# Performance work log

Measured on AMD Instinct MI355X. Metric: run time of the kernel, lower is better.

Reference implementation:

```python
import jax, jax.numpy as jnp
import numpy as np

B, G1, S, GS, D, T, H = 64, 128, 32, 16, 384, 10, 6
HD = D // H
SCALE = HD ** -0.5
GELU = lambda v: jax.nn.gelu(v, approximate=False)


def layer_norm(v, g, b, eps=1e-5):
    m = jnp.mean(v, -1, keepdims=True)
    s = jnp.mean((v - m) ** 2, -1, keepdims=True)
    return (v - m) * jax.lax.rsqrt(s + eps) * g + b


def mha(xn, qkv_w, proj_w, proj_b):
    Bc, N, C = xn.shape
    qkv = (xn @ qkv_w.T).reshape(Bc, N, 3, H, HD)
    qkv = jnp.transpose(qkv, (2, 0, 3, 1, 4))  # [3,B,H,N,hd]
    q, k, v = qkv[0], qkv[1], qkv[2]
    attn = jax.nn.softmax(jnp.einsum('bhnd,bhmd->bhnm', q, k) * SCALE, axis=-1)
    o = jnp.einsum('bhnm,bhmd->bhnd', attn, v)
    o = jnp.transpose(o, (0, 2, 1, 3)).reshape(Bc, N, C)
    return o @ proj_w.T + proj_b, attn


def propagate(xyz1, xyz2, points1, points2, de_neighbors):
    # squared pairwise distances [B,N,S]
    d = jnp.sum((xyz1[:, :, None, :] - xyz2[:, None, :, :]) ** 2, -1)
    order = jnp.argsort(d, axis=-1)[..., :de_neighbors]
    dists = jnp.take_along_axis(d, order, axis=-1)
    w = 1.0 / (dists + 1e-8)
    w = w / jnp.sum(w, -1, keepdims=True)
    gathered = jax.vmap(lambda p, i: p[i])(points2, order)  # [B,N,de,Dp]
    interp = jnp.sum(gathered * w[..., None], axis=2)
    return points1 + 0.3 * interp


def setup_inputs() -> dict:
    key = jax.random.key(0)
    ks = iter(jax.random.split(key, 64))
    rn = lambda sh, sc=1.0: jax.random.normal(next(ks), sh, jnp.float32) * sc
    w = 0.02
    inp = dict(
        x=rn((B, G1 + 1, D)),
        mask=jnp.zeros((B, G1, G1), jnp.float32),
        center1=rn((B, G1, 3)),
        center2=rn((B, S, 3)),
        neighborhood=rn((B, S, GS, 3)),
        idx=jax.random.randint(next(ks), (B * S * GS,), 0, B * (G1 + T)),
        center_idx=jax.random.randint(next(ks), (B * S,), 0, B * (G1 + T)),
        group_size=GS,
        layer_id=3,
        ln1_g=jnp.ones((D,)), ln1_b=jnp.zeros((D,)),
        ln2_g=jnp.ones((D,)), ln2_b=jnp.zeros((D,)),
        qkv_w=rn((3 * D, D), w), proj_w=rn((D, D), w), proj_b=jnp.zeros((D,)),
        fc1_w=rn((4 * D, D), w), fc1_b=jnp.zeros((4 * D,)),
        fc2_w=rn((D, 4 * D), w), fc2_b=jnp.zeros((D,)),
        ad_down_w=rn((16, D), w), ad_down_b=jnp.zeros((16,)),
        ad_up_w=rn((D, 16), w), ad_up_b=jnp.zeros((D,)),
        ad1_down_w=rn((16, D), w), ad1_down_b=jnp.zeros((16,)),
        ad1_up_w=rn((D, 16), w), ad1_up_b=jnp.zeros((D,)),
        prompt_emb=rn((T, D), w),
        bn_g=jnp.ones((D,)), bn_b=jnp.zeros((D,)),
        bn_mean=jnp.zeros((D,)), bn_var=jnp.ones((D,)),
        qkv1_w=rn((3 * D, D), w), proj1_w=rn((D, D), w), proj1_b=jnp.zeros((D,)),
        ln3_g=jnp.ones((D,)), ln3_b=jnp.zeros((D,)),
    )
    return inp


def block_forward(x, mask, center1, center2, neighborhood, idx, center_idx,
                  group_size, layer_id,
                  ln1_g, ln1_b, ln2_g, ln2_b, qkv_w, proj_w, proj_b,
                  fc1_w, fc1_b, fc2_w, fc2_b,
                  ad_down_w, ad_down_b, ad_up_w, ad_up_b,
                  ad1_down_w, ad1_down_b, ad1_up_w, ad1_up_b,
                  prompt_emb, bn_g, bn_b, bn_mean, bn_var,
                  qkv1_w, proj1_w, proj1_b, ln3_g, ln3_b):
    Bc = x.shape[0]
    # mask padding (built but unused by Attention, matching the source)
    # layer_id <= 5 branch (layer_id=3)
    prompt = jnp.broadcast_to(prompt_emb[None], (Bc, T, D))  # dropout off (eval)
    x = jnp.concatenate([x[:, :1], prompt, x[:, 1:]], axis=1)  # [B, 1+T+G1, D]
    x_fn, attn_weight = mha(layer_norm(x, ln1_g, ln1_b), qkv_w, proj_w, proj_b)
    x = x_fn + x
    xn2 = layer_norm(x, ln2_g, ln2_b)
    x_fn = GELU(xn2 @ fc1_w.T + fc1_b) @ fc2_w.T + fc2_b
    # AdapterSuper_f: bottleneck down-GELU-up (no internal residual)
    ad = GELU(x_fn @ ad_down_w.T + ad_down_b) @ ad_up_w.T + ad_up_b
    x = 0.7 * ad + x_fn + x
    prompt = x[:, 1:T + 1]
    x = jnp.concatenate([x[:, :1], x[:, T + 1:]], axis=1)  # [B, 1+G1, D]
    cls_x = x[:, 0]
    x = x[:, 1:]  # [B, G1, D]
    G = G1 + T
    prompt_x = jnp.concatenate([prompt, x], axis=1).reshape(Bc * G, D)
    x_neigh = prompt_x[idx].reshape(Bc * S, group_size, D)
    x_centers = prompt_x[center_idx].reshape(Bc, S, D)
    _ = neighborhood / (jnp.std(neighborhood) + 1e-5)  # dead in source
    # local attention over each neighborhood group
    xn3 = layer_norm(x_neigh, ln3_g, ln3_b)
    attn1_out, _a = mha(xn3, qkv1_w, proj1_w, proj1_b)
    x_neigh = attn1_out + x_neigh
    # pooling: max over group, then eval BatchNorm1d + GELU over channel dim
    lc = jnp.max(x_neigh.reshape(Bc, S, group_size, D), axis=2)  # [B,S,D]
    lc = (lc - bn_mean) * jax.lax.rsqrt(bn_var + 1e-5) * bn_g + bn_b
    lc = GELU(lc)
    vis_x = lc + 0.3 * x_centers
    x = propagate(center1, center2, x, vis_x, S)
    x = jnp.concatenate([cls_x[:, None], prompt, x], axis=1)  # [B, 1+T+G1, D]
    # AdapterSuper: bottleneck with internal residual
    x = GELU(x @ ad1_down_w.T + ad1_down_b) @ ad1_up_w.T + ad1_up_b + x
    x = jnp.concatenate([x[:, :1], x[:, T + 1:]], axis=1)  # [B, 1+G1, D]
    return x, attn_weight


def reference(x, mask, center1, center2, neighborhood, idx, center_idx,
              group_size, layer_id,
              ln1_g, ln1_b, ln2_g, ln2_b, qkv_w, proj_w, proj_b,
              fc1_w, fc1_b, fc2_w, fc2_b,
              ad_down_w, ad_down_b, ad_up_w, ad_up_b,
              ad1_down_w, ad1_down_b, ad1_up_w, ad1_up_b,
              prompt_emb, bn_g, bn_b, bn_mean, bn_var,
              qkv1_w, proj1_w, proj1_b, ln3_g, ln3_b):
    return block_forward(x, mask, center1, center2, neighborhood, idx, center_idx,
                         group_size, layer_id,
                         ln1_g, ln1_b, ln2_g, ln2_b, qkv_w, proj_w, proj_b,
                         fc1_w, fc1_b, fc2_w, fc2_b,
                         ad_down_w, ad_down_b, ad_up_w, ad_up_b,
                         ad1_down_w, ad1_down_b, ad1_up_w, ad1_up_b,
                         prompt_emb, bn_g, bn_b, bn_mean, bn_var,
                         qkv1_w, proj1_w, proj1_b, ln3_g, ln3_b)
```

## Files before the change

kernel.cpp:

```cpp
#include <hip/hip_runtime.h>
#include <hip/hip_bf16.h>

typedef __hip_bfloat16 bf16;
typedef __attribute__((ext_vector_type(8))) short short8;
typedef __attribute__((ext_vector_type(4))) float f32x4;

#define DEV static __device__ __forceinline__

DEV float b2f(bf16 v) { return __bfloat162float(v); }
DEV bf16 f2b(float v) { return __float2bfloat16(v); }
DEV unsigned short f2bu(float v) { return __builtin_bit_cast(unsigned short, __float2bfloat16(v)); }
DEV float u2f(unsigned short u) { return __uint_as_float(((unsigned int)u) << 16); }
DEV float gelu(float x) { return 0.5f * x * (1.0f + erff(x * 0.70710678118654752f)); }

#define BB 64
#define NT 139
#define DD 384
#define TT 10
#define HH 6
#define GG 138
#define M1 8896
#define MG 8832
#define NGRP 2048
#define SCALE 0.125f

#define XC_OFF   0UL
#define VIS_OFF  13664256UL
#define XNB_OFF  16809984UL
#define XFN_OFF  23642112UL
#define T16_OFF  37306368UL
#define BIG1_OFF 37875712UL
#define BIG2_OFF 58372096UL
#define ATT_OFF  XNB_OFF
#define WB_OFF   85700608UL

#define WB_QKV   0
#define WB_PROJ  442368
#define WB_FC1   589824
#define WB_FC2   1179648
#define WB_QKV1  1769472
#define WB_PROJ1 2211840
#define WB_TOTAL 2359296

#define OUT_X 3170304

DEV float4 ld4(const float* p) { return *(const float4*)p; }
DEV float4 ld4(const bf16* p) {
    ushort4 u = *(const ushort4*)p;
    return make_float4(u2f(u.x), u2f(u.y), u2f(u.z), u2f(u.w));
}
DEV void stc(float* p, float v) { *p = v; }
DEV void stc(bf16* p, float v) { *p = f2b(v); }

__global__ __launch_bounds__(256) void k_wconv(const float* __restrict__ w0, const float* __restrict__ w1,
                                               const float* __restrict__ w2, const float* __restrict__ w3,
                                               const float* __restrict__ w4, const float* __restrict__ w5,
                                               bf16* __restrict__ dst) {
    int i4 = (blockIdx.x * 256 + threadIdx.x) * 4;
    if (i4 >= WB_TOTAL) return;
    const float* s; int off;
    if (i4 < WB_PROJ)       { s = w0; off = WB_QKV; }
    else if (i4 < WB_FC1)   { s = w1; off = WB_PROJ; }
    else if (i4 < WB_FC2)   { s = w2; off = WB_FC1; }
    else if (i4 < WB_QKV1)  { s = w3; off = WB_FC2; }
    else if (i4 < WB_PROJ1) { s = w4; off = WB_QKV1; }
    else                    { s = w5; off = WB_PROJ1; }
    float4 v = *(const float4*)(s + (i4 - off));
    ushort4 u;
    u.x = f2bu(v.x); u.y = f2bu(v.y); u.z = f2bu(v.z); u.w = f2bu(v.w);
    *(ushort4*)((unsigned short*)dst + i4) = u;
}

__global__ __launch_bounds__(256) void k_build_xc(const float* __restrict__ x,
                                                  const float* __restrict__ pe,
                                                  float* __restrict__ xc) {
    int i = blockIdx.x * 256 + threadIdx.x;
    if (i >= M1 * DD) return;
    int d = i % DD, r = i / DD, n = r % NT, b = r / NT;
    float v;
    if (n == 0)        v = x[(b * 129) * DD + d];
    else if (n <= TT)  v = pe[(n - 1) * DD + d];
    else               v = x[(b * 129 + n - TT) * DD + d];
    xc[i] = v;
}

__global__ __launch_bounds__(128) void k_layernorm(const float* __restrict__ src, bf16* __restrict__ dst,
                                                   const float* __restrict__ g, const float* __restrict__ bta,
                                                   int mode) {
    int r = blockIdx.x;
    int srow = r;
    if (mode) srow = (r / GG) * NT + 1 + (r % GG);
    const float* p = src + (size_t)srow * DD;
    int t = threadIdx.x;
    float v0 = p[t], v1 = p[t + 128], v2 = p[t + 256];
    __shared__ float red[4];
    float s = v0 + v1 + v2;
    for (int off = 32; off; off >>= 1) s += __shfl_down(s, off, 64);
    if ((t & 63) == 0) red[t >> 6] = s;
    __syncthreads();
    float mean = (red[0] + red[1]) * (1.0f / 384.0f);
    float d0 = v0 - mean, d1 = v1 - mean, d2 = v2 - mean;
    float s2 = d0 * d0 + d1 * d1 + d2 * d2;
    for (int off = 32; off; off >>= 1) s2 += __shfl_down(s2, off, 64);
    if ((t & 63) == 0) red[2 + (t >> 6)] = s2;
    __syncthreads();
    float rstd = rsqrtf((red[2] + red[3]) * (1.0f / 384.0f) + 1e-5f);
    bf16* q = dst + (size_t)r * DD;
    q[t]       = f2b(d0 * rstd * g[t]       + bta[t]);
    q[t + 128] = f2b(d1 * rstd * g[t + 128] + bta[t + 128]);
    q[t + 256] = f2b(d2 * rstd * g[t + 256] + bta[t + 256]);
}

template <typename TC>
__global__ __launch_bounds__(256) void mf_gemm(const bf16* __restrict__ A, const bf16* __restrict__ W,
                                               const float* __restrict__ bias, const float* __restrict__ res,
                                               TC* __restrict__ C, int M, int N, int K, int act) {
    __shared__ bf16 As[64][72];
    __shared__ bf16 Ws[64][72];
    int t = threadIdx.x;
    int m0 = blockIdx.y * 64, n0 = blockIdx.x * 64;
    int lane = t & 63, wv = t >> 6;
    int wm = (wv >> 1) * 32, wn = (wv & 1) * 32;
    int fr = lane & 15, fq = lane >> 4;
    int sr = t >> 2, sc = (t & 3) * 16;
    const bf16* pa = A + (size_t)(m0 + sr) * K + sc;
    const bf16* pw = W + (size_t)(n0 + sr) * K + sc;
    uint4 ra0 = *(const uint4*)pa;
    uint4 ra1 = *(const uint4*)(pa + 8);
    uint4 rw0 = *(const uint4*)pw;
    uint4 rw1 = *(const uint4*)(pw + 8);
    f32x4 acc[2][2] = {};
    int k0 = 0;
    for (;;) {
        *(uint4*)&As[sr][sc] = ra0; *(uint4*)&As[sr][sc + 8] = ra1;
        *(uint4*)&Ws[sr][sc] = rw0; *(uint4*)&Ws[sr][sc + 8] = rw1;
        __syncthreads();
        k0 += 64;
        bool more = (k0 < K);
        if (more) {
            ra0 = *(const uint4*)(pa + k0); ra1 = *(const uint4*)(pa + k0 + 8);
            rw0 = *(const uint4*)(pw + k0); rw1 = *(const uint4*)(pw + k0 + 8);
        }
#pragma unroll
        for (int ks = 0; ks < 2; ++ks) {
            short8 a0 = *(const short8*)&As[wm + fr][ks * 32 + fq * 8];
            short8 a1 = *(const short8*)&As[wm + 16 + fr][ks * 32 + fq * 8];
            short8 b0 = *(const short8*)&Ws[wn + fr][ks * 32 + fq * 8];
            short8 b1 = *(const short8*)&Ws[wn + 16 + fr][ks * 32 + fq * 8];
            acc[0][0] = __builtin_amdgcn_mfma_f32_16x16x32_bf16(a0, b0, acc[0][0], 0, 0, 0);
            acc[0][1] = __builtin_amdgcn_mfma_f32_16x16x32_bf16(a0, b1, acc[0][1], 0, 0, 0);
            acc[1][0] = __builtin_amdgcn_mfma_f32_16x16x32_bf16(a1, b0, acc[1][0], 0, 0, 0);
            acc[1][1] = __builtin_amdgcn_mfma_f32_16x16x32_bf16(a1, b1, acc[1][1], 0, 0, 0);
        }
        if (!more) break;
        __syncthreads();
    }
#pragma unroll
    for (int i = 0; i < 2; ++i) {
#pragma unroll
        for (int r = 0; r < 4; ++r) {
            int row = m0 + wm + i * 16 + fq * 4 + r;
            size_t ro = (size_t)row * N;
#pragma unroll
            for (int j = 0; j < 2; ++j) {
                int col = n0 + wn + j * 16 + fr;
                float c = acc[i][j][r];
                if (bias) c += bias[col];
                if (act == 1) c = gelu(c);
                if (res) c += res[ro + col];
                stc(&C[ro + col], c);
            }
        }
    }
}

#define BM 64
#define BN 64
#define BKK 16
template <typename TA, typename TC>
__global__ __launch_bounds__(256) void k_gemm(const TA* __restrict__ A, const float* __restrict__ W,
                                              const float* __restrict__ bias, const float* __restrict__ res,
                                              TC* __restrict__ C, int M, int N, int K, int act) {
    __shared__ float As[BKK][BM + 4];
    __shared__ float Wsm[BKK][BN + 4];
    int t = threadIdx.x;
    int tx = t & 15, ty = t >> 4;
    int m0 = blockIdx.y * BM, n0 = blockIdx.x * BN;
    int lr = t >> 2;
    int lk = (t & 3) * 4;
    float acc[4][4] = {};
    for (int k0 = 0; k0 < K; k0 += BKK) {
        float4 av = ld4(A + (size_t)(m0 + lr) * K + k0 + lk);
        As[lk + 0][lr] = av.x; As[lk + 1][lr] = av.y;
        As[lk + 2][lr] = av.z; As[lk + 3][lr] = av.w;
        int wrr = n0 + lr;
        float4 wv = make_float4(0.f, 0.f, 0.f, 0.f);
        if (wrr < N) wv = ld4(W + (size_t)wrr * K + k0 + lk);
        Wsm[lk + 0][lr] = wv.x; Wsm[lk + 1][lr] = wv.y;
        Wsm[lk + 2][lr] = wv.z; Wsm[lk + 3][lr] = wv.w;
        __syncthreads();
#pragma unroll
        for (int k = 0; k < BKK; ++k) {
            float a0 = As[k][ty * 4 + 0], a1 = As[k][ty * 4 + 1];
            float a2 = As[k][ty * 4 + 2], a3 = As[k][ty * 4 + 3];
            float b0 = Wsm[k][tx * 4 + 0], b1 = Wsm[k][tx * 4 + 1];
            float b2 = Wsm[k][tx * 4 + 2], b3 = Wsm[k][tx * 4 + 3];
            acc[0][0] += a0 * b0; acc[0][1] += a0 * b1; acc[0][2] += a0 * b2; acc[0][3] += a0 * b3;
            acc[1][0] += a1 * b0; acc[1][1] += a1 * b1; acc[1][2] += a1 * b2; acc[1][3] += a1 * b3;
            acc[2][0] += a2 * b0; acc[2][1] += a2 * b1; acc[2][2] += a2 * b2; acc[2][3] += a2 * b3;
            acc[3][0] += a3 * b0; acc[3][1] += a3 * b1; acc[3][2] += a3 * b2; acc[3][3] += a3 * b3;
        }
        __syncthreads();
    }
#pragma unroll
    for (int i = 0; i < 4; ++i) {
        int m = m0 + ty * 4 + i;
        size_t ro = (size_t)m * N;
#pragma unroll
        for (int j = 0; j < 4; ++j) {
            int n = n0 + tx * 4 + j;
            if (n < N) {
                float c = acc[i][j];
                if (bias) c += bias[n];
                if (act == 1) c = gelu(c);
                if (res) c += res[ro + n];
                stc(&C[ro + n], c);
            }
        }
    }
}

__global__ __launch_bounds__(256) void k_attn1(const bf16* __restrict__ qkv, bf16* __restrict__ o_out,
                                               float* __restrict__ attn_out) {
    int bh = blockIdx.x;
    int b = bh / HH, h = bh % HH;
    __shared__ unsigned short Kl[144][72];
    __shared__ unsigned short Vt[64][160];
    __shared__ unsigned short Pl[4][16][160];
    int t = threadIdx.x;
    int lane = t & 63, wv = t >> 6;
    int fr = lane & 15, fq = lane >> 4;
    const unsigned short* q16 = (const unsigned short*)qkv;
    size_t base = (size_t)b * NT * 1152;

    uint4 z4 = make_uint4(0, 0, 0, 0);
    for (int i = t * 8; i < 64 * 160; i += 2048) *(uint4*)(&Vt[0][0] + i) = z4;
    for (int i = t * 8; i < 4 * 16 * 160; i += 2048) *(uint4*)(&Pl[0][0][0] + i) = z4;
    for (int i = t; i < 144 * 8; i += 256) {
        int row = i >> 3, ch = (i & 7) * 8;
        uint4 v = z4;
        if (row < NT) v = *(const uint4*)(q16 + base + row * 1152 + 384 + h * 64 + ch);
        *(uint4*)&Kl[row][ch] = v;
    }
    for (int i = t; i < NT * 16; i += 256) {
        int m = i >> 4, dq = (i & 15) * 4;
        ushort4 v = *(const ushort4*)(q16 + base + m * 1152 + 768 + h * 64 + dq);
        Vt[dq + 0][m] = v.x; Vt[dq + 1][m] = v.y;
        Vt[dq + 2][m] = v.z; Vt[dq + 3][m] = v.w;
    }
    __syncthreads();

    for (int nt = wv; nt < 9; nt += 4) {
        int n0 = nt * 16;
        int arow = n0 + fr; if (arow > NT - 1) arow = NT - 1;
        const unsigned short* qp = q16 + base + (size_t)arow * 1152 + h * 64 + fq * 8;
        short8 a0 = *(const short8*)qp;
        short8 a1 = *(const short8*)(qp + 32);
        f32x4 s[9] = {};
#pragma unroll
        for (int mt = 0; mt < 9; ++mt) {
            short8 b0 = *(const short8*)&Kl[mt * 16 + fr][fq * 8];
            short8 b1 = *(const short8*)&Kl[mt * 16 + fr][32 + fq * 8];
            s[mt] = __builtin_amdgcn_mfma_f32_16x16x32_bf16(a0, b0, s[mt], 0, 0, 0);
            s[mt] = __builtin_amdgcn_mfma_f32_16x16x32_bf16(a1, b1, s[mt], 0, 0, 0);
        }
#pragma unroll
        for (int r = 0; r < 4; ++r) {
            float e[9];
            float mx = -1e30f;
#pragma unroll
            for (int mt = 0; mt < 9; ++mt) {
                int col = mt * 16 + fr;
                float v = (col < NT) ? s[mt][r] * SCALE : -1e30f;
                e[mt] = v;
                mx = fmaxf(mx, v);
            }
#pragma unroll
            for (int off = 1; off < 16; off <<= 1) mx = fmaxf(mx, __shfl_xor(mx, off, 64));
            float sm = 0.f;
#pragma unroll
            for (int mt = 0; mt < 9; ++mt) { e[mt] = __expf(e[mt] - mx); sm += e[mt]; }
#pragma unroll
            for (int off = 1; off < 16; off <<= 1) sm += __shfl_xor(sm, off, 64);
            float inv = 1.0f / sm;
            int n = n0 + fq * 4 + r;
            bool nv = n < NT;
            size_t ab = ((size_t)(b * HH + h) * NT + n) * NT;
#pragma unroll
            for (int mt = 0; mt < 9; ++mt) {
                float p = e[mt] * inv;
                int col = mt * 16 + fr;
                if (nv && col < NT) attn_out[ab + col] = p;
                Pl[wv][fq * 4 + r][col] = f2bu(p);
            }
        }
        __syncthreads();
        f32x4 oac[4] = {};
#pragma unroll
        for (int ks = 0; ks < 5; ++ks) {
            short8 ap = *(const short8*)&Pl[wv][fr][ks * 32 + fq * 8];
#pragma unroll
            for (int dt = 0; dt < 4; ++dt) {
                short8 bv = *(const short8*)&Vt[dt * 16 + fr][ks * 32 + fq * 8];
                oac[dt] = __builtin_amdgcn_mfma_f32_16x16x32_bf16(ap, bv, oac[dt], 0, 0, 0);
            }
        }
#pragma unroll
        for (int dt = 0; dt < 4; ++dt)
#pragma unroll
            for (int r = 0; r < 4; ++r) {
                int n = n0 + fq * 4 + r;
                if (n < NT)
                    o_out[((size_t)(b * NT + n)) * DD + h * 64 + dt * 16 + fr] = f2b(oac[dt][r]);
            }
    }
}

__global__ __launch_bounds__(64) void k_attn2(const bf16* __restrict__ qkv, const int* __restrict__ idx,
                                              bf16* __restrict__ o1) {
    int g = blockIdx.x;
    __shared__ unsigned short Vt2[64][40];
    __shared__ unsigned short P2[16][40];
    __shared__ int ridx[16];
    int t = threadIdx.x;
    int fr = t & 15, fq = t >> 4;
    const unsigned short* q16 = (const unsigned short*)qkv;
    if (t < 16) ridx[t] = idx[g * 16 + t];
    uint4 z4 = make_uint4(0, 0, 0, 0);
    for (int i = t * 8; i < 64 * 40; i += 512) *(uint4*)(&Vt2[0][0] + i) = z4;
    for (int i = t * 8; i < 16 * 40; i += 512) *(uint4*)(&P2[0][0] + i) = z4;
    __syncthreads();
    size_t qb = (size_t)ridx[fr] * 1152;
    for (int h = 0; h < HH; ++h) {
        for (int i = t; i < 256; i += 64) {
            int m = i >> 4, dq = (i & 15) * 4;
            ushort4 v = *(const ushort4*)(q16 + (size_t)ridx[m] * 1152 + 768 + h * 64 + dq);
            Vt2[dq + 0][m] = v.x; Vt2[dq + 1][m] = v.y;
            Vt2[dq + 2][m] = v.z; Vt2[dq + 3][m] = v.w;
        }
        __syncthreads();
        const unsigned short* qp = q16 + qb + h * 64 + fq * 8;
        const unsigned short* kp = q16 + qb + 384 + h * 64 + fq * 8;
        short8 a0 = *(const short8*)qp;
        short8 a1 = *(const short8*)(qp + 32);
        short8 b0 = *(const short8*)kp;
        short8 b1 = *(const short8*)(kp + 32);
        f32x4 s = {};
        s = __builtin_amdgcn_mfma_f32_16x16x32_bf16(a0, b0, s, 0, 0, 0);
        s = __builtin_amdgcn_mfma_f32_16x16x32_bf16(a1, b1, s, 0, 0, 0);
#pragma unroll
        for (int r = 0; r < 4; ++r) {
            float v = s[r] * SCALE;
            float mx = v;
#pragma unroll
            for (int off = 1; off < 16; off <<= 1) mx = fmaxf(mx, __shfl_xor(mx, off, 64));
            float e = __expf(v - mx), sm = e;
#pragma unroll
            for (int off = 1; off < 16; off <<= 1) sm += __shfl_xor(sm, off, 64);
            P2[fq * 4 + r][fr] = f2bu(e / sm);
        }
        __syncthreads();
        short8 ap = *(const short8*)&P2[fr][fq * 8];
        f32x4 oac[4] = {};
#pragma unroll
        for (int dt = 0; dt < 4; ++dt) {
            short8 bv = *(const short8*)&Vt2[dt * 16 + fr][fq * 8];
            oac[dt] = __builtin_amdgcn_mfma_f32_16x16x32_bf16(ap, bv, oac[dt], 0, 0, 0);
        }
#pragma unroll
        for (int dt = 0; dt < 4; ++dt)
#pragma unroll
            for (int r = 0; r < 4; ++r)
                o1[((size_t)(g * 16 + fq * 4 + r)) * DD + h * 64 + dt * 16 + fr] = f2b(oac[dt][r]);
        __syncthreads();
    }
}

__global__ __launch_bounds__(128) void k_ad_combine(const float* __restrict__ t16, const float* __restrict__ upw,
                                                    const float* __restrict__ upb, const float* __restrict__ xfn,
                                                    float* xc) {
    int r = blockIdx.x, t = threadIdx.x;
    __shared__ float tl[16];
    if (t < 16) tl[t] = t16[r * 16 + t];
    __syncthreads();
    for (int d = t; d < DD; d += 128) {
        float acc = 0.f;
#pragma unroll
        for (int c = 0; c < 4; ++c) {
            float4 u = *(const float4*)(upw + d * 16 + c * 4);
            acc += tl[c * 4 + 0] * u.x + tl[c * 4 + 1] * u.y
                 + tl[c * 4 + 2] * u.z + tl[c * 4 + 3] * u.w;
        }
        acc += upb[d];
        size_t i = (size_t)r * DD + d;
        xc[i] += 0.7f * acc + xfn[i];
    }
}

__global__ __launch_bounds__(128) void k_groupmax(const bf16* __restrict__ att, const float* __restrict__ xc,
                                                  const int* __restrict__ idx, const int* __restrict__ cidx,
                                                  const float* __restrict__ bg, const float* __restrict__ bb,
                                                  const float* __restrict__ bmean, const float* __restrict__ bvar,
                                                  float* __restrict__ vis) {
    int g = blockIdx.x, t = threadIdx.x;
    __shared__ int rows[16];
    __shared__ int crow;
    if (t < 16) { int r = idx[g * 16 + t]; rows[t] = (r / GG) * NT + 1 + (r % GG); }
    if (t == 16) { int r = cidx[g]; crow = (r / GG) * NT + 1 + (r % GG); }
    __syncthreads();
    for (int d = t; d < DD; d += 128) {
        float m = -INFINITY;
#pragma unroll
        for (int j = 0; j < 16; ++j) {
            float v = b2f(att[((size_t)(g * 16 + j)) * DD + d]) + xc[(size_t)rows[j] * DD + d];
            m = fmaxf(m, v);
        }
        float bn = (m - bmean[d]) * rsqrtf(bvar[d] + 1e-5f) * bg[d] + bb[d];
        bn = gelu(bn);
        vis[(size_t)g * DD + d] = bn + 0.3f * xc[(size_t)crow * DD + d];
    }
}

__global__ __launch_bounds__(128) void k_propagate(const float* __restrict__ c1, const float* __restrict__ c2,
                                                   const float* __restrict__ xc, const float* __restrict__ vis,
                                                   float* __restrict__ xp) {
    int blk = blockIdx.x;
    int b = blk >> 7, i = blk & 127;
    int t = threadIdx.x;
    __shared__ float wl[32];
    __shared__ float wsum;
    if (t < 32) {
        float dx = c1[(b * 128 + i) * 3 + 0] - c2[(b * 32 + t) * 3 + 0];
        float dy = c1[(b * 128 + i) * 3 + 1] - c2[(b * 32 + t) * 3 + 1];
        float dz = c1[(b * 128 + i) * 3 + 2] - c2[(b * 32 + t) * 3 + 2];
        wl[t] = 1.0f / (dx * dx + dy * dy + dz * dz + 1e-8f);
    }
    __syncthreads();
    if (t == 0) {
        float s = 0.f;
        for (int j = 0; j < 32; ++j) s += wl[j];
        wsum = s;
    }
    __syncthreads();
    float sc = 0.3f / wsum;
    for (int d = t; d < DD; d += 128) {
        float acc = 0.f;
#pragma unroll 8
        for (int j = 0; j < 32; ++j) acc += wl[j] * vis[((size_t)(b * 32 + j)) * DD + d];
        xp[((size_t)(b * 128 + i)) * DD + d] = xc[((size_t)(b * NT + 11 + i)) * DD + d] + sc * acc;
    }
}

__global__ __launch_bounds__(256) void k_build_xfinal(const float* __restrict__ xc, const float* __restrict__ xp,
                                                      float* __restrict__ xf) {
    int i = blockIdx.x * 256 + threadIdx.x;
    if (i >= M1 * DD) return;
    int d = i % DD, r = i / DD, n = r % NT, b = r / NT;
    xf[i] = (n < 11) ? xc[i] : xp[((size_t)(b * 128 + n - 11)) * DD + d];
}

__global__ __launch_bounds__(128) void k_final(const float* __restrict__ t16, const float* __restrict__ upw,
                                               const float* __restrict__ upb, const float* __restrict__ xf,
                                               float* __restrict__ outx) {
    int rb = blockIdx.x, t = threadIdx.x;
    int b = rb / 129, no = rb % 129;
    int src = b * NT + (no == 0 ? 0 : no + TT);
    __shared__ float tl[16];
    if (t < 16) tl[t] = t16[src * 16 + t];
    __syncthreads();
    for (int d = t; d < DD; d += 128) {
        float acc = 0.f;
#pragma unroll
        for (int c = 0; c < 4; ++c) {
            float4 u = *(const float4*)(upw + d * 16 + c * 4);
            acc += tl[c * 4 + 0] * u.x + tl[c * 4 + 1] * u.y
                 + tl[c * 4 + 2] * u.z + tl[c * 4 + 3] * u.w;
        }
        acc += upb[d];
        outx[(size_t)rb * DD + d] = acc + xf[(size_t)src * DD + d];
    }
}

extern "C" void kernel_launch(void* const* d_in, const int* in_sizes, int n_in,
                              void* d_out, int out_size, void* d_ws, size_t ws_size,
                              hipStream_t stream) {
    const float* x_in    = (const float*)d_in[0];
    const float* center1 = (const float*)d_in[2];
    const float* center2 = (const float*)d_in[3];
    const int*   idx     = (const int*)d_in[5];
    const int*   cidx    = (const int*)d_in[6];
    const float* ln1_g   = (const float*)d_in[9];
    const float* ln1_b   = (const float*)d_in[10];
    const float* ln2_g   = (const float*)d_in[11];
    const float* ln2_b   = (const float*)d_in[12];
    const float* qkv_w   = (const float*)d_in[13];
    const float* proj_w  = (const float*)d_in[14];
    const float* proj_b  = (const float*)d_in[15];
    const float* fc1_w   = (const float*)d_in[16];
    const float* fc1_b   = (const float*)d_in[17];
    const float* fc2_w   = (const float*)d_in[18];
    const float* fc2_b   = (const float*)d_in[19];
    const float* ad_dw   = (const float*)d_in[20];
    const float* ad_db   = (const float*)d_in[21];
    const float* ad_uw   = (const float*)d_in[22];
    const float* ad_ub   = (const float*)d_in[23];
    const float* ad1_dw  = (const float*)d_in[24];
    const float* ad1_db  = (const float*)d_in[25];
    const float* ad1_uw  = (const float*)d_in[26];
    const float* ad1_ub  = (const float*)d_in[27];
    const float* prompt  = (const float*)d_in[28];
    const float* bn_g    = (const float*)d_in[29];
    const float* bn_b    = (const float*)d_in[30];
    const float* bn_mean = (const float*)d_in[31];
    const float* bn_var  = (const float*)d_in[32];
    const float* qkv1_w  = (const float*)d_in[33];
    const float* proj1_w = (const float*)d_in[34];
    const float* proj1_b = (const float*)d_in[35];
    const float* ln3_g   = (const float*)d_in[36];
    const float* ln3_b   = (const float*)d_in[37];

    char* wsb = (char*)d_ws;
    float* XC   = (float*)(wsb + XC_OFF);
    float* VIS  = (float*)(wsb + VIS_OFF);
    bf16*  XNB  = (bf16*)(wsb + XNB_OFF);
    float* XFN  = (float*)(wsb + XFN_OFF);
    float* T16  = (float*)(wsb + T16_OFF);
    bf16*  BIG1 = (bf16*)(wsb + BIG1_OFF);
    bf16*  BIG2 = (bf16*)(wsb + BIG2_OFF);
    float* XFIN = (float*)(wsb + BIG2_OFF);
    bf16*  ATT  = (bf16*)(wsb + ATT_OFF);
    bf16*  WB   = (bf16*)(wsb + WB_OFF);

    float* out_x    = (float*)d_out;
    float* out_attn = out_x + OUT_X;

    k_wconv<<<(WB_TOTAL / 4 + 255) / 256, 256, 0, stream>>>(qkv_w, proj_w, fc1_w, fc2_w, qkv1_w, proj1_w, WB);

    k_build_xc<<<(M1 * DD + 255) / 256, 256, 0, stream>>>(x_in, prompt, XC);
    k_layernorm<<<M1, 128, 0, stream>>>(XC, XNB, ln1_g, ln1_b, 0);
    mf_gemm<<<dim3(18, 139), 256, 0, stream>>>(XNB, WB + WB_QKV, (const float*)nullptr, (const float*)nullptr, BIG1, M1, 1152, 384, 0);
    k_attn1<<<BB * HH, 256, 0, stream>>>(BIG1, XNB, out_attn);
    mf_gemm<<<dim3(6, 139), 256, 0, stream>>>(XNB, WB + WB_PROJ, proj_b, XC, XC, M1, 384, 384, 0);
    k_layernorm<<<M1, 128, 0, stream>>>(XC, XNB, ln2_g, ln2_b, 0);
    mf_gemm<<<dim3(24, 139), 256, 0, stream>>>(XNB, WB + WB_FC1, fc1_b, (const float*)nullptr, BIG2, M1, 1536, 384, 1);
    mf_gemm<<<dim3(6, 139), 256, 0, stream>>>(BIG2, WB + WB_FC2, fc2_b, (const float*)nullptr, XFN, M1, 384, 1536, 0);
    k_gemm<<<dim3(1, 139), 256, 0, stream>>>(XFN, ad_dw, ad_db, (const float*)nullptr, T16, M1, 16, 384, 1);
    k_ad_combine<<<M1, 128, 0, stream>>>(T16, ad_uw, ad_ub, XFN, XC);

    k_layernorm<<<MG, 128, 0, stream>>>(XC, XNB, ln3_g, ln3_b, 1);
    mf_gemm<<<dim3(18, 138), 256, 0, stream>>>(XNB, WB + WB_QKV1, (const float*)nullptr, (const float*)nullptr, BIG1, MG, 1152, 384, 0);
    k_attn2<<<NGRP, 64, 0, stream>>>(BIG1, idx, BIG2);
    mf_gemm<<<dim3(6, 512), 256, 0, stream>>>(BIG2, WB + WB_PROJ1, proj1_b, (const float*)nullptr, ATT, NGRP * 16, 384, 384, 0);
    k_groupmax<<<NGRP, 128, 0, stream>>>(ATT, XC, idx, cidx, bn_g, bn_b, bn_mean, bn_var, VIS);
    k_propagate<<<BB * 128, 128, 0, stream>>>(center1, center2, XC, VIS, XFN);

    k_build_xfinal<<<(M1 * DD + 255) / 256, 256, 0, stream>>>(XC, XFN, XFIN);
    k_gemm<<<dim3(1, 139), 256, 0, stream>>>(XFIN, ad1_dw, ad1_db, (const float*)nullptr, T16, M1, 16, 384, 1);
    k_final<<<BB * 129, 128, 0, stream>>>(T16, ad1_uw, ad1_ub, XFIN, out_x);
}
```

Measured before the change: 498.6 us.

## Fuse input build into LN1 and merge adapter down/up passes into single kernels

Folds the concat-build of the token matrix into the first layernorm kernel, which now writes the fp32 residual copy and the normalized bf16 rows in one pass. Replaces each adapter's separate down-projection GEMM plus up-projection/combine kernel with one kernel that stages 16 rows in shared memory and does both projections and the residual update. The final adapter also gathers the kept tokens directly, so the intermediate full matrix build and the extra copy pass go away. This saves several launches and full-matrix round trips through global memory. The cost is a scalar per-thread 384-long dot product that reads the down weights from global memory.

```diff
diff --git a/kernel.cpp b/kernel.cpp
--- a/kernel.cpp
+++ b/kernel.cpp
@@ -28,7 +28,6 @@
 #define VIS_OFF  13664256UL
 #define XNB_OFF  16809984UL
 #define XFN_OFF  23642112UL
-#define T16_OFF  37306368UL
 #define BIG1_OFF 37875712UL
 #define BIG2_OFF 58372096UL
 #define ATT_OFF  XNB_OFF
@@ -45,10 +44,6 @@
 #define OUT_X 3170304
 
 DEV float4 ld4(const float* p) { return *(const float4*)p; }
-DEV float4 ld4(const bf16* p) {
-    ushort4 u = *(const ushort4*)p;
-    return make_float4(u2f(u.x), u2f(u.y), u2f(u.z), u2f(u.w));
-}
 DEV void stc(float* p, float v) { *p = v; }
 DEV void stc(bf16* p, float v) { *p = f2b(v); }
 
@@ -71,17 +66,35 @@
     *(ushort4*)((unsigned short*)dst + i4) = u;
 }
 
-__global__ __launch_bounds__(256) void k_build_xc(const float* __restrict__ x,
-                                                  const float* __restrict__ pe,
-                                                  float* __restrict__ xc) {
-    int i = blockIdx.x * 256 + threadIdx.x;
-    if (i >= M1 * DD) return;
-    int d = i % DD, r = i / DD, n = r % NT, b = r / NT;
-    float v;
-    if (n == 0)        v = x[(b * 129) * DD + d];
-    else if (n <= TT)  v = pe[(n - 1) * DD + d];
-    else               v = x[(b * 129 + n - TT) * DD + d];
-    xc[i] = v;
+__global__ __launch_bounds__(128) void k_ln1(const float* __restrict__ x, const float* __restrict__ pe,
+                                             const float* __restrict__ g, const float* __restrict__ bta,
+                                             float* __restrict__ xc, bf16* __restrict__ dst) {
+    int r = blockIdx.x;
+    int b = r / NT, n = r % NT;
+    const float* p;
+    if (n == 0)       p = x + (size_t)(b * 129) * DD;
+    else if (n <= TT) p = pe + (size_t)(n - 1) * DD;
+    else              p = x + (size_t)(b * 129 + n - TT) * DD;
+    int t = threadIdx.x;
+    float v0 = p[t], v1 = p[t + 128], v2 = p[t + 256];
+    float* xq = xc + (size_t)r * DD;
+    xq[t] = v0; xq[t + 128] = v1; xq[t + 256] = v2;
+    __shared__ float red[4];
+    float s = v0 + v1 + v2;
+    for (int off = 32; off; off >>= 1) s += __shfl_down(s, off, 64);
+    if ((t & 63) == 0) red[t >> 6] = s;
+    __syncthreads();
+    float mean = (red[0] + red[1]) * (1.0f / 384.0f);
+    float d0 = v0 - mean, d1 = v1 - mean, d2 = v2 - mean;
+    float s2 = d0 * d0 + d1 * d1 + d2 * d2;
+    for (int off = 32; off; off >>= 1) s2 += __shfl_down(s2, off, 64);
+    if ((t & 63) == 0) red[2 + (t >> 6)] = s2;
+    __syncthreads();
+    float rstd = rsqrtf((red[2] + red[3]) * (1.0f / 384.0f) + 1e-5f);
+    bf16* q = dst + (size_t)r * DD;
+    q[t]       = f2b(d0 * rstd * g[t]       + bta[t]);
+    q[t + 128] = f2b(d1 * rstd * g[t + 128] + bta[t + 128]);
+    q[t + 256] = f2b(d2 * rstd * g[t + 256] + bta[t + 256]);
 }
 
 __global__ __launch_bounds__(128) void k_layernorm(const float* __restrict__ src, bf16* __restrict__ dst,
@@ -174,59 +187,88 @@
     }
 }
 
-#define BM 64
-#define BN 64
-#define BKK 16
-template <typename TA, typename TC>
-__global__ __launch_bounds__(256) void k_gemm(const TA* __restrict__ A, const float* __restrict__ W,
-                                              const float* __restrict__ bias, const float* __restrict__ res,
-                                              TC* __restrict__ C, int M, int N, int K, int act) {
-    __shared__ float As[BKK][BM + 4];
-    __shared__ float Wsm[BKK][BN + 4];
-    int t = threadIdx.x;
-    int tx = t & 15, ty = t >> 4;
-    int m0 = blockIdx.y * BM, n0 = blockIdx.x * BN;
-    int lr = t >> 2;
-    int lk = (t & 3) * 4;
-    float acc[4][4] = {};
-    for (int k0 = 0; k0 < K; k0 += BKK) {
-        float4 av = ld4(A + (size_t)(m0 + lr) * K + k0 + lk);
-        As[lk + 0][lr] = av.x; As[lk + 1][lr] = av.y;
-        As[lk + 2][lr] = av.z; As[lk + 3][lr] = av.w;
-        int wrr = n0 + lr;
-        float4 wv = make_float4(0.f, 0.f, 0.f, 0.f);
-        if (wrr < N) wv = ld4(W + (size_t)wrr * K + k0 + lk);
-        Wsm[lk + 0][lr] = wv.x; Wsm[lk + 1][lr] = wv.y;
-        Wsm[lk + 2][lr] = wv.z; Wsm[lk + 3][lr] = wv.w;
-        __syncthreads();
-#pragma unroll
-        for (int k = 0; k < BKK; ++k) {
-            float a0 = As[k][ty * 4 + 0], a1 = As[k][ty * 4 + 1];
-            float a2 = As[k][ty * 4 + 2], a3 = As[k][ty * 4 + 3];
-            float b0 = Wsm[k][tx * 4 + 0], b1 = Wsm[k][tx * 4 + 1];
-            float b2 = Wsm[k][tx * 4 + 2], b3 = Wsm[k][tx * 4 + 3];
-            acc[0][0] += a0 * b0; acc[0][1] += a0 * b1; acc[0][2] += a0 * b2; acc[0][3] += a0 * b3;
-            acc[1][0] += a1 * b0; acc[1][1] += a1 * b1; acc[1][2] += a1 * b2; acc[1][3] += a1 * b3;
-            acc[2][0] += a2 * b0; acc[2][1] += a2 * b1; acc[2][2] += a2 * b2; acc[2][3] += a2 * b3;
-            acc[3][0] += a3 * b0; acc[3][1] += a3 * b1; acc[3][2] += a3 * b2; acc[3][3] += a3 * b3;
-        }
-        __syncthreads();
-    }
-#pragma unroll
-    for (int i = 0; i < 4; ++i) {
-        int m = m0 + ty * 4 + i;
-        size_t ro = (size_t)m * N;
-#pragma unroll
-        for (int j = 0; j < 4; ++j) {
-            int n = n0 + tx * 4 + j;
-            if (n < N) {
-                float c = acc[i][j];
-                if (bias) c += bias[n];
-                if (act == 1) c = gelu(c);
-                if (res) c += res[ro + n];
-                stc(&C[ro + n], c);
-            }
-        }
+__global__ __launch_bounds__(256) void k_adapter1(const float* __restrict__ xfn, const float* __restrict__ dw,
+                                                  const float* __restrict__ db, const float* __restrict__ uw,
+                                                  const float* __restrict__ ub, float* __restrict__ xc) {
+    __shared__ float S[16][400];
+    __shared__ float Tl[16][16];
+    int t = threadIdx.x;
+    int r0 = blockIdx.x * 16;
+    for (int i = t * 4; i < 16 * 384; i += 1024) {
+        int rr = i / 384, cc = i - rr * 384;
+        *(float4*)&S[rr][cc] = *(const float4*)(xfn + (size_t)(r0 + rr) * DD + cc);
+    }
+    __syncthreads();
+    int r = t >> 4, c = t & 15;
+    float acc = db[c];
+    const float* wp = dw + c * 384;
+    for (int k = 0; k < 384; k += 4) {
+        float4 sv = *(const float4*)&S[r][k];
+        float4 wvv = *(const float4*)(wp + k);
+        acc += sv.x * wvv.x + sv.y * wvv.y + sv.z * wvv.z + sv.w * wvv.w;
+    }
+    Tl[r][c] = gelu(acc);
+    __syncthreads();
+    float tr[16];
+#pragma unroll
+    for (int j = 0; j < 4; ++j) *(float4*)&tr[j * 4] = *(const float4*)&Tl[r][j * 4];
+    size_t rowoff = (size_t)(r0 + r) * DD;
+#pragma unroll 4
+    for (int j = 0; j < 24; ++j) {
+        int d = c + j * 16;
+        float a = ub[d];
+        const float4* up4 = (const float4*)(uw + d * 16);
+        float4 u0 = up4[0], u1 = up4[1], u2 = up4[2], u3 = up4[3];
+        a += tr[0] * u0.x + tr[1] * u0.y + tr[2] * u0.z + tr[3] * u0.w
+           + tr[4] * u1.x + tr[5] * u1.y + tr[6] * u1.z + tr[7] * u1.w
+           + tr[8] * u2.x + tr[9] * u2.y + tr[10] * u2.z + tr[11] * u2.w
+           + tr[12] * u3.x + tr[13] * u3.y + tr[14] * u3.z + tr[15] * u3.w;
+        xc[rowoff + d] += 0.7f * a + S[r][d];
+    }
+}
+
+__global__ __launch_bounds__(256) void k_adapter2(const float* __restrict__ xc, const float* __restrict__ xp,
+                                                  const float* __restrict__ dw, const float* __restrict__ db,
+                                                  const float* __restrict__ uw, const float* __restrict__ ub,
+                                                  float* __restrict__ outx) {
+    __shared__ float S[16][400];
+    __shared__ float Tl[16][16];
+    int t = threadIdx.x;
+    int r0 = blockIdx.x * 16;
+    for (int i = t * 4; i < 16 * 384; i += 1024) {
+        int rr = i / 384, cc = i - rr * 384;
+        int gidx = r0 + rr;
+        int b = gidx / 129, no = gidx - b * 129;
+        const float* src = (no == 0) ? (xc + (size_t)(b * NT) * DD)
+                                     : (xp + (size_t)(b * 128 + no - 1) * DD);
+        *(float4*)&S[rr][cc] = *(const float4*)(src + cc);
+    }
+    __syncthreads();
+    int r = t >> 4, c = t & 15;
+    float acc = db[c];
+    const float* wp = dw + c * 384;
+    for (int k = 0; k < 384; k += 4) {
+        float4 sv = *(const float4*)&S[r][k];
+        float4 wvv = *(const float4*)(wp + k);
+        acc += sv.x * wvv.x + sv.y * wvv.y + sv.z * wvv.z + sv.w * wvv.w;
+    }
+    Tl[r][c] = gelu(acc);
+    __syncthreads();
+    float tr[16];
+#pragma unroll
+    for (int j = 0; j < 4; ++j) *(float4*)&tr[j * 4] = *(const float4*)&Tl[r][j * 4];
+    size_t rowoff = (size_t)(r0 + r) * DD;
+#pragma unroll 4
+    for (int j = 0; j < 24; ++j) {
+        int d = c + j * 16;
+        float a = ub[d];
+        const float4* up4 = (const float4*)(uw + d * 16);
+        float4 u0 = up4[0], u1 = up4[1], u2 = up4[2], u3 = up4[3];
+        a += tr[0] * u0.x + tr[1] * u0.y + tr[2] * u0.z + tr[3] * u0.w
+           + tr[4] * u1.x + tr[5] * u1.y + tr[6] * u1.z + tr[7] * u1.w
+           + tr[8] * u2.x + tr[9] * u2.y + tr[10] * u2.z + tr[11] * u2.w
+           + tr[12] * u3.x + tr[13] * u3.y + tr[14] * u3.z + tr[15] * u3.w;
+        outx[rowoff + d] = a + S[r][d];
     }
 }
 
@@ -386,27 +428,6 @@
     }
 }
 
-__global__ __launch_bounds__(128) void k_ad_combine(const float* __restrict__ t16, const float* __restrict__ upw,
-                                                    const float* __restrict__ upb, const float* __restrict__ xfn,
-                                                    float* xc) {
-    int r = blockIdx.x, t = threadIdx.x;
-    __shared__ float tl[16];
-    if (t < 16) tl[t] = t16[r * 16 + t];
-    __syncthreads();
-    for (int d = t; d < DD; d += 128) {
-        float acc = 0.f;
-#pragma unroll
-        for (int c = 0; c < 4; ++c) {
-            float4 u = *(const float4*)(upw + d * 16 + c * 4);
-            acc += tl[c * 4 + 0] * u.x + tl[c * 4 + 1] * u.y
-                 + tl[c * 4 + 2] * u.z + tl[c * 4 + 3] * u.w;
-        }
-        acc += upb[d];
-        size_t i = (size_t)r * DD + d;
-        xc[i] += 0.7f * acc + xfn[i];
-    }
-}
-
 __global__ __launch_bounds__(128) void k_groupmax(const bf16* __restrict__ att, const float* __restrict__ xc,
                                                   const int* __restrict__ idx, const int* __restrict__ cidx,
                                                   const float* __restrict__ bg, const float* __restrict__ bb,
@@ -458,36 +479,6 @@
 #pragma unroll 8
         for (int j = 0; j < 32; ++j) acc += wl[j] * vis[((size_t)(b * 32 + j)) * DD + d];
         xp[((size_t)(b * 128 + i)) * DD + d] = xc[((size_t)(b * NT + 11 + i)) * DD + d] + sc * acc;
-    }
-}
-
-__global__ __launch_bounds__(256) void k_build_xfinal(const float* __restrict__ xc, const float* __restrict__ xp,
-                                                      float* __restrict__ xf) {
-    int i = blockIdx.x * 256 + threadIdx.x;
-    if (i >= M1 * DD) return;
-    int d = i % DD, r = i / DD, n = r % NT, b = r / NT;
-    xf[i] = (n < 11) ? xc[i] : xp[((size_t)(b * 128 + n - 11)) * DD + d];
-}
-
-__global__ __launch_bounds__(128) void k_final(const float* __restrict__ t16, const float* __restrict__ upw,
-                                               const float* __restrict__ upb, const float* __restrict__ xf,
-                                               float* __restrict__ outx) {
-    int rb = blockIdx.x, t = threadIdx.x;
-    int b = rb / 129, no = rb % 129;
-    int src = b * NT + (no == 0 ? 0 : no + TT);
-    __shared__ float tl[16];
-    if (t < 16) tl[t] = t16[src * 16 + t];
-    __syncthreads();
-    for (int d = t; d < DD; d += 128) {
-        float acc = 0.f;
-#pragma unroll
-        for (int c = 0; c < 4; ++c) {
-            float4 u = *(const float4*)(upw + d * 16 + c * 4);
-            acc += tl[c * 4 + 0] * u.x + tl[c * 4 + 1] * u.y
-                 + tl[c * 4 + 2] * u.z + tl[c * 4 + 3] * u.w;
-        }
-        acc += upb[d];
-        outx[(size_t)rb * DD + d] = acc + xf[(size_t)src * DD + d];
     }
 }
 
@@ -534,10 +525,8 @@
     float* VIS  = (float*)(wsb + VIS_OFF);
     bf16*  XNB  = (bf16*)(wsb + XNB_OFF);
     float* XFN  = (float*)(wsb + XFN_OFF);
-    float* T16  = (float*)(wsb + T16_OFF);
     bf16*  BIG1 = (bf16*)(wsb + BIG1_OFF);
     bf16*  BIG2 = (bf16*)(wsb + BIG2_OFF);
-    float* XFIN = (float*)(wsb + BIG2_OFF);
     bf16*  ATT  = (bf16*)(wsb + ATT_OFF);
     bf16*  WB   = (bf16*)(wsb + WB_OFF);
 
@@ -546,16 +535,14 @@
 
     k_wconv<<<(WB_TOTAL / 4 + 255) / 256, 256, 0, stream>>>(qkv_w, proj_w, fc1_w, fc2_w, qkv1_w, proj1_w, WB);
 
-    k_build_xc<<<(M1 * DD + 255) / 256, 256, 0, stream>>>(x_in, prompt, XC);
-    k_layernorm<<<M1, 128, 0, stream>>>(XC, XNB, ln1_g, ln1_b, 0);
+    k_ln1<<<M1, 128, 0, stream>>>(x_in, prompt, ln1_g, ln1_b, XC, XNB);
     mf_gemm<<<dim3(18, 139), 256, 0, stream>>>(XNB, WB + WB_QKV, (const float*)nullptr, (const float*)nullptr, BIG1, M1, 1152, 384, 0);
     k_attn1<<<BB * HH, 256, 0, stream>>>(BIG1, XNB, out_attn);
     mf_gemm<<<dim3(6, 139), 256, 0, stream>>>(XNB, WB + WB_PROJ, proj_b, XC, XC, M1, 384, 384, 0);
     k_layernorm<<<M1, 128, 0, stream>>>(XC, XNB, ln2_g, ln2_b, 0);
     mf_gemm<<<dim3(24, 139), 256, 0, stream>>>(XNB, WB + WB_FC1, fc1_b, (const float*)nullptr, BIG2, M1, 1536, 384, 1);
     mf_gemm<<<dim3(6, 139), 256, 0, stream>>>(BIG2, WB + WB_FC2, fc2_b, (const float*)nullptr, XFN, M1, 384, 1536, 0);
-    k_gemm<<<dim3(1, 139), 256, 0, stream>>>(XFN, ad_dw, ad_db, (const float*)nullptr, T16, M1, 16, 384, 1);
-    k_ad_combine<<<M1, 128, 0, stream>>>(T16, ad_uw, ad_ub, XFN, XC);
+    k_adapter1<<<M1 / 16, 256, 0, stream>>>(XFN, ad_dw, ad_db, ad_uw, ad_ub, XC);
 
     k_layernorm<<<MG, 128, 0, stream>>>(XC, XNB, ln3_g, ln3_b, 1);
     mf_gemm<<<dim3(18, 138), 256, 0, stream>>>(XNB, WB + WB_QKV1, (const float*)nullptr, (const float*)nullptr, BIG1, MG, 1152, 384, 0);
@@ -564,7 +551,5 @@
     k_groupmax<<<NGRP, 128, 0, stream>>>(ATT, XC, idx, cidx, bn_g, bn_b, bn_mean, bn_var, VIS);
     k_propagate<<<BB * 128, 128, 0, stream>>>(center1, center2, XC, VIS, XFN);
 
-    k_build_xfinal<<<(M1 * DD + 255) / 256, 256, 0, stream>>>(XC, XFN, XFIN);
-    k_gemm<<<dim3(1, 139), 256, 0, stream>>>(XFIN, ad1_dw, ad1_db, (const float*)nullptr, T16, M1, 16, 384, 1);
-    k_final<<<BB * 129, 128, 0, stream>>>(T16, ad1_uw, ad1_ub, XFIN, out_x);
-}
+    k_adapter2<<<(BB * 129) / 16, 256, 0, stream>>>(XC, XFN, ad1_dw, ad1_db, ad1_uw, ad1_ub, out_x);
+}
```

After: 508.9 us. 2.1% more time.
